# Performance work log

Hardware: AMD Instinct MI355X
Metric: run time of the kernel (lower is better)

The kernel has to match this reference:

```python
import jax, jax.numpy as jnp
import numpy as np

N_AGENTS, N_ENEMIES, N_ACTIONS = 8, 8, 14
ALLY_F, ENEMY_F = 8, 6
EMBED, RNN, HYPEMB, HYPHID = 32, 64, 64, 64
STATE_DIM = N_AGENTS * ALLY_F + N_ENEMIES * ENEMY_F + N_AGENTS * N_ACTIONS  # 224


def setup_inputs() -> dict:
    key = jax.random.key(0)
    ks = jax.random.split(key, 16)
    b, t = 64, 256
    rn = lambda k, s, sc=0.05: jax.random.normal(k, s, jnp.float32) * sc
    return dict(
        qvals=rn(ks[0], (b, t, N_AGENTS), 1.0),
        states=rn(ks[1], (b, t, STATE_DIM), 1.0),
        hidden_states=rn(ks[2], (b, t, N_AGENTS, RNN), 1.0),
        hw1_w=rn(ks[3], (RNN, EMBED)), hw1_b=jnp.zeros((EMBED,), jnp.float32),
        en_h1w=rn(ks[4], (ENEMY_F, HYPHID)), en_h1b=jnp.zeros((HYPHID,), jnp.float32),
        en_h2w=rn(ks[5], (HYPHID, ENEMY_F * HYPEMB)), en_h2b=jnp.zeros((ENEMY_F * HYPEMB,), jnp.float32),
        en_bias=jnp.zeros((1, HYPEMB), jnp.float32),
        al_h1w=rn(ks[6], (ALLY_F, HYPHID)), al_h1b=jnp.zeros((HYPHID,), jnp.float32),
        al_h2w=rn(ks[7], (HYPHID, ALLY_F * HYPEMB)), al_h2b=jnp.zeros((ALLY_F * HYPEMB,), jnp.float32),
        al_bias=jnp.zeros((1, HYPEMB), jnp.float32),
        act_w=rn(ks[8], (N_ACTIONS, HYPEMB)), act_b=jnp.zeros((HYPEMB,), jnp.float32),
        hb1_w=rn(ks[9], (HYPEMB, EMBED)), hb1_b=jnp.zeros((EMBED,), jnp.float32),
        hw2_w=rn(ks[10], (HYPEMB, EMBED)), hw2_b=jnp.zeros((EMBED,), jnp.float32),
        hb2_w=rn(ks[11], (HYPEMB, 1)), hb2_b=jnp.zeros((1,), jnp.float32),
    )


def _hyperlinear(x, h1w, h1b, h2w, h2b, bias, din, dout):
    # hypernet MLP -> per-sample weight matrix [rows, din, dout]
    h = jax.nn.relu(x @ h1w + h1b)
    W = (h @ h2w + h2b).reshape(-1, din, dout)
    return jnp.einsum('bi,bio->bo', x, W) + bias


def reference(qvals, states, hidden_states, hw1_w, hw1_b,
              en_h1w, en_h1b, en_h2w, en_h2b, en_bias,
              al_h1w, al_h1b, al_h2w, al_h2b, al_bias,
              act_w, act_b, hb1_w, hb1_b, hw2_w, hw2_b, hb2_w, hb2_b):
    b, t, _ = qvals.shape
    BT = b * t
    s = states.reshape(BT, STATE_DIM)
    ally = s[:, :N_AGENTS * ALLY_F].reshape(-1, ALLY_F)                # [BT*A, 8]
    enemy = s[:, N_AGENTS * ALLY_F:N_AGENTS * ALLY_F + N_ENEMIES * ENEMY_F].reshape(-1, ENEMY_F)
    actions = s[:, N_AGENTS * ALLY_F + N_ENEMIES * ENEMY_F:].reshape(BT, N_AGENTS, N_ACTIONS)

    embed_ally = _hyperlinear(ally, al_h1w, al_h1b, al_h2w, al_h2b, al_bias,
                              ALLY_F, HYPEMB).reshape(BT, N_AGENTS, HYPEMB).mean(axis=1)
    embed_enemy = _hyperlinear(enemy, en_h1w, en_h1b, en_h2w, en_h2b, en_bias,
                               ENEMY_F, HYPEMB).reshape(BT, N_ENEMIES, HYPEMB).mean(axis=1)
    embed_action = (actions @ act_w + act_b).mean(axis=1)
    se = jax.nn.relu(embed_ally + embed_enemy + embed_action)          # [BT, HYPEMB]

    w1 = jax.nn.softmax((hidden_states @ hw1_w + hw1_b).reshape(BT, N_AGENTS, EMBED), axis=1)
    b1 = (se @ hb1_w + hb1_b).reshape(BT, 1, EMBED)
    w2 = jnp.abs(se @ hw2_w + hw2_b).reshape(BT, EMBED, 1)
    b2 = (se @ hb2_w + hb2_b).reshape(BT, 1, 1)

    q = qvals.reshape(BT, 1, N_AGENTS)
    hidden = jax.nn.elu(jnp.matmul(q, w1) + b1)                        # [BT, 1, EMBED]
    y = jnp.matmul(hidden, w2) + b2                                    # [BT, 1, 1]
    return y.reshape(b, t, 1)
```

## Files before the change

kernel.cpp:

```cpp
#include <hip/hip_runtime.h>
#include <hip/hip_bf16.h>
#include <stdint.h>

typedef unsigned short u16t;
typedef float f32x4 __attribute__((ext_vector_type(4)));
typedef short bf16x8 __attribute__((ext_vector_type(8)));

#define SDIM 224

__device__ __forceinline__ float lo16(uint32_t w) { union { uint32_t u; float f; } v; v.u = w << 16; return v.f; }
__device__ __forceinline__ u16t bf1(float a) {
    union { __hip_bfloat16 h; u16t u; } c; c.h = __float2bfloat16(a); return c.u;
}
__device__ __forceinline__ uint32_t pk2(float a, float b) {
    union { __hip_bfloat162 h; uint32_t u; } c;
    c.h = __float22bfloat162_rn(make_float2(a, b));
    return c.u;
}

__global__ void prep_wt_kernel(const float* __restrict__ h2wA, const float* __restrict__ h2wB,
                               const float* __restrict__ h2bA, const float* __restrict__ h2bB,
                               const float* __restrict__ actw,
                               const float* __restrict__ hb1w, const float* __restrict__ hw2w,
                               const float* __restrict__ hw1w,
                               u16t* __restrict__ wtA, u16t* __restrict__ wtB,
                               u16t* __restrict__ wt2, u16t* __restrict__ wtM)
{
    const int t0 = blockIdx.x * 256 + threadIdx.x, stride = gridDim.x * 256;
    for (int e = t0; e < 34816; e += stride) {
        int j = e & 7, n = (e >> 3) & 63, kb = e >> 9;
        int k = kb * 8 + j;
        float v = 0.f;
        if (k < 512)      { int h = k & 63, i = k >> 6; v = h2wA[h * 512 + i * 64 + n]; }
        else if (k < 520) v = h2bA[(k - 512) * 64 + n];
        wtA[e] = bf1(v);
    }
    for (int e = t0; e < 26624; e += stride) {
        int j = e & 7, n = (e >> 3) & 63, kb = e >> 9;
        int k = kb * 8 + j;
        float v = 0.f;
        if (k < 384)      { int h = k & 63, i = k >> 6; v = h2wB[h * 384 + i * 64 + n]; }
        else if (k < 390) v = h2bB[(k - 384) * 64 + n];
        else if (k < 404) v = actw[(k - 390) * 64 + n];
        wtB[e] = bf1(v);
    }
    for (int e = t0; e < 4096; e += stride) {
        int j = e & 7, n = (e >> 3) & 63, kb = e >> 9;
        int k = kb * 8 + j;
        float v = (n < 32) ? hb1w[k * 32 + n] : hw2w[k * 32 + (n - 32)];
        wt2[e] = bf1(v);
    }
    for (int e = t0; e < 2048; e += stride) {
        int j = e & 7, n = (e >> 3) & 31, kb = e >> 8;
        wtM[e] = bf1(hw1w[(kb * 8 + j) * 32 + n]);
    }
}

template<int DIN, int KP, int FOFF>
__device__ __forceinline__ void stage1(const float (*sx)[112], u16t* __restrict__ ps,
                                       const float* __restrict__ s_h1w, float b1r,
                                       int wave, int lane)
{
    float w1r[DIN];
#pragma unroll
    for (int i = 0; i < DIN; ++i) w1r[i] = s_h1w[i * 64 + lane];
#pragma unroll 1
    for (int ss = 0; ss < 4; ++ss) {
        const int s = wave * 4 + ss;
        const float* xr = &sx[s][FOFF];
        float psv[DIN];
#pragma unroll
        for (int i = 0; i < DIN; ++i) psv[i] = 0.f;
#pragma unroll
        for (int a = 0; a < 8; ++a) {
            float x[DIN];
            if constexpr (DIN == 8) {
                float4 v0 = *(const float4*)(xr + a * 8);
                float4 v1 = *(const float4*)(xr + a * 8 + 4);
                x[0] = v0.x; x[1] = v0.y; x[2] = v0.z; x[3] = v0.w;
                x[4] = v1.x; x[5] = v1.y; x[6] = v1.z; x[7] = v1.w;
            } else {
                float2 v0 = *(const float2*)(xr + a * 6);
                float2 v1 = *(const float2*)(xr + a * 6 + 2);
                float2 v2 = *(const float2*)(xr + a * 6 + 4);
                x[0] = v0.x; x[1] = v0.y; x[2] = v1.x; x[3] = v1.y; x[4] = v2.x; x[5] = v2.y;
            }
            float hacc = b1r;
#pragma unroll
            for (int i = 0; i < DIN; ++i) hacc += x[i] * w1r[i];
            hacc = fmaxf(hacc, 0.f);
#pragma unroll
            for (int i = 0; i < DIN; ++i) psv[i] += hacc * x[i];
        }
#pragma unroll
        for (int i = 0; i < DIN; i += 2) {
            union { __hip_bfloat162 h; struct { u16t lo, hi; } w; } c;
            c.h = __float22bfloat162_rn(make_float2(psv[i], psv[i + 1]));
            ps[s * KP + i * 64 + lane]       = c.w.lo;
            ps[s * KP + (i + 1) * 64 + lane] = c.w.hi;
        }
    }
}

__global__ __launch_bounds__(256, 4)
void fused_mixer(const float* __restrict__ qvals, const float* __restrict__ states,
                 const float* __restrict__ hs,
                 const float* __restrict__ al_h1w, const float* __restrict__ al_h1b,
                 const float* __restrict__ en_h1w, const float* __restrict__ en_h1b,
                 const float* __restrict__ al_bias, const float* __restrict__ en_bias,
                 const float* __restrict__ act_b,
                 const float* __restrict__ hb1_b, const float* __restrict__ hw2_b,
                 const float* __restrict__ hw1_b, const float* __restrict__ hb2_w,
                 const float* __restrict__ hb2_b,
                 const u16t* __restrict__ wtA, const u16t* __restrict__ wtB,
                 const u16t* __restrict__ wt2, const u16t* __restrict__ wtM,
                 float* __restrict__ out)
{
    constexpr int KPA = 552, KPB = 424;
    __shared__ __align__(16) char  s_un[18432];
    __shared__ __align__(16) float s_x[16][112];
    __shared__ float s_act[16][14];
    __shared__ __align__(16) u16t  s_se[16 * 72];
    __shared__ float s_b1w2[16][64];
    __shared__ float s_b2[16];
    __shared__ float s_q[128];
    __shared__ float s_h1wA[512], s_h1wB[384];
    __shared__ float s_h1bA[64], s_h1bB[64], s_bias3[64], s_hb2w[64];
    __shared__ float s_b1b[32], s_w2b[32], s_w1b[32];
    __shared__ float s_hb2bv;

    const int tid  = threadIdx.x;
    const int wave = tid >> 6;
    const int lane = tid & 63;
    const int lr = lane & 15, lg = lane >> 4;
    const int sbase = blockIdx.x * 16;
    const int o = wave * 16 + lr;

    for (int i = tid; i < 16 * 28; i += 256) {
        int s = i / 28, c = i - s * 28;
        *(float4*)&s_x[s][c * 4] = *(const float4*)(states + (size_t)(sbase + s) * SDIM + c * 4);
    }
    if (tid < 224) {
        int s = tid / 14, j = tid - s * 14;
        const float* ap = states + (size_t)(sbase + s) * SDIM + 112 + j;
        float t = 0.f;
#pragma unroll
        for (int a = 0; a < 8; ++a) t += ap[a * 14];
        s_act[s][j] = t;
    }
    for (int i = tid; i < 512; i += 256) s_h1wA[i] = al_h1w[i];
    for (int i = tid; i < 384; i += 256) s_h1wB[i] = en_h1w[i];
    if (tid < 64) {
        s_h1bA[tid] = al_h1b[tid]; s_h1bB[tid] = en_h1b[tid];
        s_bias3[tid] = al_bias[tid] + en_bias[tid] + act_b[tid];
        s_hb2w[tid] = hb2_w[tid];
    }
    if (tid >= 64 && tid < 96)   s_b1b[tid - 64] = hb1_b[tid - 64];
    if (tid >= 96 && tid < 128)  s_w2b[tid - 96] = hw2_b[tid - 96];
    if (tid >= 128 && tid < 160) s_w1b[tid - 128] = hw1_b[tid - 128];
    if (tid >= 160 && tid < 288 - 32) {  }
    if (tid == 160) s_hb2bv = hb2_b[0];
    if (tid >= 128 && tid < 256 && tid - 128 < 128) s_q[tid - 128] = qvals[(size_t)sbase * 8 + (tid - 128)];
    __syncthreads();

    u16t* ps = (u16t*)s_un;

    stage1<8, KPA, 0>(s_x, ps, s_h1wA, s_h1bA[lane], wave, lane);
    if (tid < 128) {
        int s = tid >> 3, i = tid & 7;
        float t = 0.f;
#pragma unroll
        for (int a = 0; a < 8; ++a) t += s_x[s][a * 8 + i];
        ps[s * KPA + 512 + i] = bf1(t);
    } else {
        int idx = tid - 128;
        for (int u = idx; u < 192; u += 128) {
            int s = u / 12, r = u - s * 12;
            *(uint32_t*)&ps[s * KPA + 520 + r * 2] = 0u;
        }
    }
    __syncthreads();

    f32x4 accA = {0.f, 0.f, 0.f, 0.f};
    {
        const u16t* arow = ps + lr * KPA + lg * 8;
        const bf16x8* wt8 = (const bf16x8*)wtA;
#pragma unroll 4
        for (int kk = 0; kk < 544; kk += 32) {
            bf16x8 av = *(const bf16x8*)(arow + kk);
            bf16x8 bv = wt8[((kk >> 3) + lg) * 64 + o];
            accA = __builtin_amdgcn_mfma_f32_16x16x32_bf16(av, bv, accA, 0, 0, 0);
        }
    }
    __syncthreads();

    float4 hsr[8];
    {
        const float4* hsv = (const float4*)(hs + (size_t)sbase * 512);
#pragma unroll
        for (int i = 0; i < 8; ++i) hsr[i] = hsv[i * 256 + tid];
    }
    stage1<6, KPB, 64>(s_x, ps, s_h1wB, s_h1bB[lane], wave, lane);
    if (tid < 96) {
        int s = tid / 6, i = tid - s * 6;
        float t = 0.f;
#pragma unroll
        for (int a = 0; a < 8; ++a) t += s_x[s][64 + a * 6 + i];
        ps[s * KPB + 384 + i] = bf1(t);
    } else {
        int idx = tid - 96;
        for (int u = idx; u < 224; u += 160) {
            int s = u / 14, j = u - s * 14;
            ps[s * KPB + 390 + j] = bf1(s_act[s][j]);
        }
    }
    if (tid < 96) {
        int s = tid / 6, r = tid - (tid / 6) * 6;
        *(uint32_t*)&ps[s * KPB + 404 + r * 2] = 0u;
    }
    __syncthreads();

    {
        f32x4 accB = {0.f, 0.f, 0.f, 0.f};
        const u16t* arow = ps + lr * KPB + lg * 8;
        const bf16x8* wt8 = (const bf16x8*)wtB;
#pragma unroll 4
        for (int kk = 0; kk < 416; kk += 32) {
            bf16x8 av = *(const bf16x8*)(arow + kk);
            bf16x8 bv = wt8[((kk >> 3) + lg) * 64 + o];
            accB = __builtin_amdgcn_mfma_f32_16x16x32_bf16(av, bv, accB, 0, 0, 0);
        }
#pragma unroll
        for (int j = 0; j < 4; ++j) {
            const int row = lg * 4 + j;
            float se = (accA[j] + accB[j]) * 0.125f + s_bias3[o];
            s_se[row * 72 + o] = bf1(fmaxf(se, 0.f));
        }
    }
    __syncthreads();

    u16t* s_hs = (u16t*)s_un;
    {
#pragma unroll
        for (int i = 0; i < 8; ++i) {
            const int idx = i * 256 + tid;
            const int row = idx >> 4, c4 = idx & 15;
            uint2 p;
            p.x = pk2(hsr[i].x, hsr[i].y);
            p.y = pk2(hsr[i].z, hsr[i].w);
            *(uint2*)&s_hs[row * 72 + c4 * 4] = p;
        }
    }
    {
        f32x4 acc = {0.f, 0.f, 0.f, 0.f};
        const u16t* serow = &s_se[lr * 72 + lg * 8];
        const bf16x8* wt8 = (const bf16x8*)wt2;
#pragma unroll
        for (int ks = 0; ks < 2; ++ks) {
            bf16x8 av = *(const bf16x8*)(serow + ks * 32);
            bf16x8 bv = wt8[(ks * 4 + lg) * 64 + o];
            acc = __builtin_amdgcn_mfma_f32_16x16x32_bf16(av, bv, acc, 0, 0, 0);
        }
#pragma unroll
        for (int j = 0; j < 4; ++j) {
            const int row = lg * 4 + j;
            float v = acc[j] + ((o < 32) ? s_b1b[o] : s_w2b[o - 32]);
            if (o >= 32) v = fabsf(v);
            s_b1w2[row][o] = v;
        }
    }
    {
        const int smp = wave * 4 + lg;
        float p = 0.f;
#pragma unroll
        for (int c = 0; c < 4; ++c) {
            const int oo = c * 16 + lr;
            p += lo16((uint32_t)s_se[smp * 72 + oo]) * s_hb2w[oo];
        }
        p += __shfl_xor(p, 1); p += __shfl_xor(p, 2);
        p += __shfl_xor(p, 4); p += __shfl_xor(p, 8);
        if (lr == 0) s_b2[smp] = p + s_hb2bv;
    }
    __syncthreads();

    bf16x8 bfr[2][2];
    {
        const bf16x8* wtm8 = (const bf16x8*)wtM;
#pragma unroll
        for (int n = 0; n < 2; ++n)
#pragma unroll
            for (int ks = 0; ks < 2; ++ks)
                bfr[n][ks] = wtm8[(ks * 4 + lg) * 32 + n * 16 + lr];
    }
    const float zb0 = s_w1b[lr], zb1 = s_w1b[16 + lr];

    for (int t = wave * 2; t < wave * 2 + 2; ++t) {
        f32x4 d0 = {0.f,0.f,0.f,0.f}, d1 = {0.f,0.f,0.f,0.f};
#pragma unroll
        for (int ks = 0; ks < 2; ++ks) {
            bf16x8 av = *(const bf16x8*)&s_hs[(t * 16 + lr) * 72 + ks * 32 + lg * 8];
            d0 = __builtin_amdgcn_mfma_f32_16x16x32_bf16(av, bfr[0][ks], d0, 0, 0, 0);
            d1 = __builtin_amdgcn_mfma_f32_16x16x32_bf16(av, bfr[1][ks], d1, 0, 0, 0);
        }
        const int sloc = t * 2 + (lg >> 1);
        float z0[4], z1[4];
#pragma unroll
        for (int j = 0; j < 4; ++j) { z0[j] = d0[j] + zb0; z1[j] = d1[j] + zb1; }
        float m0 = fmaxf(fmaxf(z0[0], z0[1]), fmaxf(z0[2], z0[3]));
        float m1 = fmaxf(fmaxf(z1[0], z1[1]), fmaxf(z1[2], z1[3]));
        m0 = fmaxf(m0, __shfl_xor(m0, 16));
        m1 = fmaxf(m1, __shfl_xor(m1, 16));
        float qa[4];
        {
            float4 qv = *(const float4*)&s_q[sloc * 8 + (lg & 1) * 4];
            qa[0] = qv.x; qa[1] = qv.y; qa[2] = qv.z; qa[3] = qv.w;
        }
        float s0 = 0.f, s1 = 0.f, hp0 = 0.f, hp1 = 0.f;
#pragma unroll
        for (int j = 0; j < 4; ++j) {
            float e0 = __expf(z0[j] - m0), e1 = __expf(z1[j] - m1);
            s0 += e0; s1 += e1;
            hp0 += qa[j] * e0; hp1 += qa[j] * e1;
        }
        s0  += __shfl_xor(s0, 16);  s1  += __shfl_xor(s1, 16);
        hp0 += __shfl_xor(hp0, 16); hp1 += __shfl_xor(hp1, 16);

        const float b1_0 = s_b1w2[sloc][lr],      b1_1 = s_b1w2[sloc][16 + lr];
        const float w2_0 = s_b1w2[sloc][32 + lr], w2_1 = s_b1w2[sloc][48 + lr];
        float h0 = hp0 / s0 + b1_0; h0 = (h0 > 0.f) ? h0 : (__expf(h0) - 1.f);
        float h1 = hp1 / s1 + b1_1; h1 = (h1 > 0.f) ? h1 : (__expf(h1) - 1.f);
        float yp = h0 * w2_0 + h1 * w2_1;
        yp += __shfl_xor(yp, 1); yp += __shfl_xor(yp, 2);
        yp += __shfl_xor(yp, 4); yp += __shfl_xor(yp, 8);
        if (lr == 0 && (lg & 1) == 0) out[sbase + sloc] = yp + s_b2[sloc];
    }
}

extern "C" void kernel_launch(void* const* d_in, const int* in_sizes, int n_in,
                              void* d_out, int out_size, void* d_ws, size_t ws_size,
                              hipStream_t stream) {
    const float* qvals   = (const float*)d_in[0];
    const float* states  = (const float*)d_in[1];
    const float* hstates = (const float*)d_in[2];
    const float* hw1_w   = (const float*)d_in[3];
    const float* hw1_b   = (const float*)d_in[4];
    const float* en_h1w  = (const float*)d_in[5];
    const float* en_h1b  = (const float*)d_in[6];
    const float* en_h2w  = (const float*)d_in[7];
    const float* en_h2b  = (const float*)d_in[8];
    const float* en_bias = (const float*)d_in[9];
    const float* al_h1w  = (const float*)d_in[10];
    const float* al_h1b  = (const float*)d_in[11];
    const float* al_h2w  = (const float*)d_in[12];
    const float* al_h2b  = (const float*)d_in[13];
    const float* al_bias = (const float*)d_in[14];
    const float* act_w   = (const float*)d_in[15];
    const float* act_b   = (const float*)d_in[16];
    const float* hb1_w   = (const float*)d_in[17];
    const float* hb1_b   = (const float*)d_in[18];
    const float* hw2_w   = (const float*)d_in[19];
    const float* hw2_b   = (const float*)d_in[20];
    const float* hb2_w   = (const float*)d_in[21];
    const float* hb2_b   = (const float*)d_in[22];

    u16t* wtA = (u16t*)d_ws;
    u16t* wtB = wtA + 34816;
    u16t* wt2 = wtA + 61440;
    u16t* wtM = wtA + 65536;

    prep_wt_kernel<<<64, 256, 0, stream>>>(al_h2w, en_h2w, al_h2b, en_h2b, act_w,
                                           hb1_w, hw2_w, hw1_w, wtA, wtB, wt2, wtM);
    fused_mixer<<<1024, 256, 0, stream>>>(qvals, states, hstates,
                                          al_h1w, al_h1b, en_h1w, en_h1b,
                                          al_bias, en_bias, act_b,
                                          hb1_b, hw2_b, hw1_b, hb2_w, hb2_b,
                                          wtA, wtB, wt2, wtM, (float*)d_out);
}
```

Before: 34.81 us.

## Pack stage-1 partial sums as 16-byte rows and read states directly from global

New measurement: 48.63 us. 39.7% more time.

```diff
diff --git a/kernel.cpp b/kernel.cpp
--- a/kernel.cpp
+++ b/kernel.cpp
@@ -31,17 +31,17 @@
         int j = e & 7, n = (e >> 3) & 63, kb = e >> 9;
         int k = kb * 8 + j;
         float v = 0.f;
-        if (k < 512)      { int h = k & 63, i = k >> 6; v = h2wA[h * 512 + i * 64 + n]; }
+        if (k < 512)      { int h = k >> 3, i = k & 7; v = h2wA[h * 512 + i * 64 + n]; }
         else if (k < 520) v = h2bA[(k - 512) * 64 + n];
         wtA[e] = bf1(v);
     }
-    for (int e = t0; e < 26624; e += stride) {
+    for (int e = t0; e < 34816; e += stride) {
         int j = e & 7, n = (e >> 3) & 63, kb = e >> 9;
         int k = kb * 8 + j;
         float v = 0.f;
-        if (k < 384)      { int h = k & 63, i = k >> 6; v = h2wB[h * 384 + i * 64 + n]; }
-        else if (k < 390) v = h2bB[(k - 384) * 64 + n];
-        else if (k < 404) v = actw[(k - 390) * 64 + n];
+        if (k < 512)      { int h = k >> 3, i = k & 7; if (i < 6) v = h2wB[h * 384 + i * 64 + n]; }
+        else if (k < 518) v = h2bB[(k - 512) * 64 + n];
+        else if (k < 532) v = actw[(k - 518) * 64 + n];
         wtB[e] = bf1(v);
     }
     for (int e = t0; e < 4096; e += stride) {
@@ -56,10 +56,11 @@
     }
 }
 
-template<int DIN, int KP, int FOFF>
-__device__ __forceinline__ void stage1(const float (*sx)[112], u16t* __restrict__ ps,
-                                       const float* __restrict__ s_h1w, float b1r,
-                                       int wave, int lane)
+template<int DIN>
+__device__ __forceinline__ void stage1g(const float* __restrict__ xbase,
+                                        u16t* __restrict__ ps,
+                                        const float* __restrict__ s_h1w, float b1r,
+                                        int wave, int lane)
 {
     float w1r[DIN];
 #pragma unroll
@@ -67,10 +68,10 @@
 #pragma unroll 1
     for (int ss = 0; ss < 4; ++ss) {
         const int s = wave * 4 + ss;
-        const float* xr = &sx[s][FOFF];
-        float psv[DIN];
-#pragma unroll
-        for (int i = 0; i < DIN; ++i) psv[i] = 0.f;
+        const float* xr = xbase + s * SDIM;
+        float psv[8];
+#pragma unroll
+        for (int i = 0; i < 8; ++i) psv[i] = 0.f;
 #pragma unroll
         for (int a = 0; a < 8; ++a) {
             float x[DIN];
@@ -92,13 +93,12 @@
 #pragma unroll
             for (int i = 0; i < DIN; ++i) psv[i] += hacc * x[i];
         }
-#pragma unroll
-        for (int i = 0; i < DIN; i += 2) {
-            union { __hip_bfloat162 h; struct { u16t lo, hi; } w; } c;
-            c.h = __float22bfloat162_rn(make_float2(psv[i], psv[i + 1]));
-            ps[s * KP + i * 64 + lane]       = c.w.lo;
-            ps[s * KP + (i + 1) * 64 + lane] = c.w.hi;
-        }
+        uint4 p;
+        p.x = pk2(psv[0], psv[1]);
+        p.y = pk2(psv[2], psv[3]);
+        p.z = pk2(psv[4], psv[5]);
+        p.w = (DIN == 8) ? pk2(psv[6], psv[7]) : 0u;
+        *(uint4*)&ps[s * 552 + lane * 8] = p;
     }
 }
 
@@ -116,9 +116,8 @@
                  const u16t* __restrict__ wt2, const u16t* __restrict__ wtM,
                  float* __restrict__ out)
 {
-    constexpr int KPA = 552, KPB = 424;
+    constexpr int KP = 552;
     __shared__ __align__(16) char  s_un[18432];
-    __shared__ __align__(16) float s_x[16][112];
     __shared__ float s_act[16][14];
     __shared__ __align__(16) u16t  s_se[16 * 72];
     __shared__ float s_b1w2[16][64];
@@ -135,14 +134,11 @@
     const int lr = lane & 15, lg = lane >> 4;
     const int sbase = blockIdx.x * 16;
     const int o = wave * 16 + lr;
-
-    for (int i = tid; i < 16 * 28; i += 256) {
-        int s = i / 28, c = i - s * 28;
-        *(float4*)&s_x[s][c * 4] = *(const float4*)(states + (size_t)(sbase + s) * SDIM + c * 4);
-    }
+    const float* xg = states + (size_t)sbase * SDIM;
+
     if (tid < 224) {
-        int s = tid / 14, j = tid - s * 14;
-        const float* ap = states + (size_t)(sbase + s) * SDIM + 112 + j;
+        int s = tid / 14, j = tid - (tid / 14) * 14;
+        const float* ap = xg + s * SDIM + 112 + j;
         float t = 0.f;
 #pragma unroll
         for (int a = 0; a < 8; ++a) t += ap[a * 14];
@@ -158,32 +154,32 @@
     if (tid >= 64 && tid < 96)   s_b1b[tid - 64] = hb1_b[tid - 64];
     if (tid >= 96 && tid < 128)  s_w2b[tid - 96] = hw2_b[tid - 96];
     if (tid >= 128 && tid < 160) s_w1b[tid - 128] = hw1_b[tid - 128];
-    if (tid >= 160 && tid < 288 - 32) {  }
     if (tid == 160) s_hb2bv = hb2_b[0];
-    if (tid >= 128 && tid < 256 && tid - 128 < 128) s_q[tid - 128] = qvals[(size_t)sbase * 8 + (tid - 128)];
+    if (tid >= 128) s_q[tid - 128] = qvals[(size_t)sbase * 8 + (tid - 128)];
     __syncthreads();
 
     u16t* ps = (u16t*)s_un;
 
-    stage1<8, KPA, 0>(s_x, ps, s_h1wA, s_h1bA[lane], wave, lane);
+    stage1g<8>(xg, ps, s_h1wA, s_h1bA[lane], wave, lane);
     if (tid < 128) {
         int s = tid >> 3, i = tid & 7;
+        const float* xp = xg + s * SDIM + i;
         float t = 0.f;
 #pragma unroll
-        for (int a = 0; a < 8; ++a) t += s_x[s][a * 8 + i];
-        ps[s * KPA + 512 + i] = bf1(t);
+        for (int a = 0; a < 8; ++a) t += xp[a * 8];
+        ps[s * KP + 512 + i] = bf1(t);
     } else {
         int idx = tid - 128;
         for (int u = idx; u < 192; u += 128) {
-            int s = u / 12, r = u - s * 12;
-            *(uint32_t*)&ps[s * KPA + 520 + r * 2] = 0u;
+            int s = u / 12, r = u - (u / 12) * 12;
+            *(uint32_t*)&ps[s * KP + 520 + r * 2] = 0u;
         }
     }
     __syncthreads();
 
     f32x4 accA = {0.f, 0.f, 0.f, 0.f};
     {
-        const u16t* arow = ps + lr * KPA + lg * 8;
+        const u16t* arow = ps + lr * KP + lg * 8;
         const bf16x8* wt8 = (const bf16x8*)wtA;
 #pragma unroll 4
         for (int kk = 0; kk < 544; kk += 32) {
@@ -200,32 +196,33 @@
 #pragma unroll
         for (int i = 0; i < 8; ++i) hsr[i] = hsv[i * 256 + tid];
     }
-    stage1<6, KPB, 64>(s_x, ps, s_h1wB, s_h1bB[lane], wave, lane);
+    stage1g<6>(xg + 64, ps, s_h1wB, s_h1bB[lane], wave, lane);
     if (tid < 96) {
-        int s = tid / 6, i = tid - s * 6;
+        int s = tid / 6, i = tid - (tid / 6) * 6;
+        const float* xp = xg + s * SDIM + 64 + i;
         float t = 0.f;
 #pragma unroll
-        for (int a = 0; a < 8; ++a) t += s_x[s][64 + a * 6 + i];
-        ps[s * KPB + 384 + i] = bf1(t);
+        for (int a = 0; a < 8; ++a) t += xp[a * 6];
+        ps[s * KP + 512 + i] = bf1(t);
     } else {
         int idx = tid - 96;
         for (int u = idx; u < 224; u += 160) {
-            int s = u / 14, j = u - s * 14;
-            ps[s * KPB + 390 + j] = bf1(s_act[s][j]);
+            int s = u / 14, j = u - (u / 14) * 14;
+            ps[s * KP + 518 + j] = bf1(s_act[s][j]);
         }
     }
     if (tid < 96) {
         int s = tid / 6, r = tid - (tid / 6) * 6;
-        *(uint32_t*)&ps[s * KPB + 404 + r * 2] = 0u;
+        *(uint32_t*)&ps[s * KP + 532 + r * 2] = 0u;
     }
     __syncthreads();
 
     {
         f32x4 accB = {0.f, 0.f, 0.f, 0.f};
-        const u16t* arow = ps + lr * KPB + lg * 8;
+        const u16t* arow = ps + lr * KP + lg * 8;
         const bf16x8* wt8 = (const bf16x8*)wtB;
 #pragma unroll 4
-        for (int kk = 0; kk < 416; kk += 32) {
+        for (int kk = 0; kk < 544; kk += 32) {
             bf16x8 av = *(const bf16x8*)(arow + kk);
             bf16x8 bv = wt8[((kk >> 3) + lg) * 64 + o];
             accB = __builtin_amdgcn_mfma_f32_16x16x32_bf16(av, bv, accB, 0, 0, 0);
@@ -365,8 +362,8 @@
 
     u16t* wtA = (u16t*)d_ws;
     u16t* wtB = wtA + 34816;
-    u16t* wt2 = wtA + 61440;
-    u16t* wtM = wtA + 65536;
+    u16t* wt2 = wtA + 69632;
+    u16t* wtM = wtA + 73728;
 
     prep_wt_kernel<<<64, 256, 0, stream>>>(al_h2w, en_h2w, al_h2b, en_h2b, act_w,
                                            hb1_w, hw2_w, hw1_w, wtA, wtB, wt2, wtM);
```
